# Optimization experiments

Hardware: AMD Instinct MI355X
Metric: run time of the kernel (lower is better)

## Reference

```python
import jax, jax.numpy as jnp
import numpy as np

N, E, D, K, H = 100000, 1600000, 32, 3, 1


def setup_inputs() -> dict:
    key = jax.random.key(0)
    ks = jax.random.split(key, 7)
    return {
        "src": jax.random.randint(ks[0], (E,), 0, N),
        "dst": jax.random.randint(ks[1], (E,), 0, N),
        "embedding": jax.random.normal(ks[2], (N, D), jnp.float32),
        "lambda_max": jnp.full((1,), 2.0, jnp.float32),
        # ChebConv: single Linear(k*d -> d) over concatenated Chebyshev terms (shared by both calls)
        "cheb_W": jax.random.normal(ks[3], (K * D, D), jnp.float32) / np.sqrt(K * D),
        "cheb_b": jnp.zeros((D,), jnp.float32),
        # GATv2: fc_src / fc_dst Linear(d -> H*d) + attention vector (H, d)
        "gat_W_src": jax.random.normal(ks[4], (D, H * D), jnp.float32) / np.sqrt(D),
        "gat_b_src": jnp.zeros((H * D,), jnp.float32),
        "gat_W_dst": jax.random.normal(ks[5], (D, H * D), jnp.float32) / np.sqrt(D),
        "gat_b_dst": jnp.zeros((H * D,), jnp.float32),
        "gat_attn": jax.random.normal(ks[6], (H, D), jnp.float32) / np.sqrt(D),
    }


def _cheb(src, dst, feat, lam, W, b, n):
    # DGL ChebConv with lambda_max given; activation = leaky_relu (slope 0.01)
    deg = jnp.clip(jax.ops.segment_sum(jnp.ones(src.shape[0], feat.dtype), dst, num_segments=n), 1.0)
    dinv = deg[:, None] ** -0.5  # D^{-1/2}, (N,1)
    re_norm = 2.0 / lam[0]

    def unnL(f):  # D^{-1/2} A D^{-1/2} f
        return jax.ops.segment_sum((f * dinv)[src], dst, num_segments=n) * dinv

    X0 = feat
    X1 = -re_norm * unnL(X0) + X0 * (re_norm - 1.0)
    Xs = [X0, X1]
    for _ in range(2, K):
        Xi = -2.0 * re_norm * unnL(X1) + X1 * (2.0 * (re_norm - 1.0)) - X0
        Xs.append(Xi)
        X0, X1 = X1, Xi
    return jax.nn.leaky_relu(jnp.concatenate(Xs, axis=1) @ W + b, 0.01)


def _gatv2(src, dst, h, Ws, bs, Wd, bd, attn, n):
    Hh, Dd = attn.shape
    fs = (h @ Ws + bs).reshape(n, Hh, Dd)  # feat_src 'el'
    fd = (h @ Wd + bd).reshape(n, Hh, Dd)  # feat_dst 'er'
    e = jax.nn.leaky_relu(fs[src] + fd[dst], 0.2)        # (E,H,D), GATv2 negative_slope=0.2
    logits = jnp.einsum('ehd,hd->eh', e, attn)           # (E,H)
    m = jax.ops.segment_max(logits, dst, num_segments=n)  # per-dst softmax (edge_softmax)
    ex = jnp.exp(logits - m[dst])
    a = ex / jax.ops.segment_sum(ex, dst, num_segments=n)[dst]
    ft = jax.ops.segment_sum(fs[src] * a[..., None], dst, num_segments=n)  # (N,H,D)
    return jax.nn.leaky_relu(ft, 0.01)  # activation=F.leaky_relu


def reference(src, dst, embedding, lambda_max, cheb_W, cheb_b,
              gat_W_src, gat_b_src, gat_W_dst, gat_b_dst, gat_attn):
    n, d = embedding.shape
    h = _cheb(src, dst, embedding, lambda_max, cheb_W, cheb_b, n)
    h = _cheb(src, dst, h, lambda_max, cheb_W, cheb_b, n)
    out = _gatv2(src, dst, h, gat_W_src, gat_b_src, gat_W_dst, gat_b_dst, gat_attn, n)
    return out.reshape(-1, d)
```

## Files before the change

### kernel.cpp

```cpp
#include <hip/hip_runtime.h>

#define TPB 256
#define NB 512
#define CAPB 4096
#define CHUNK 4096
#define CAPS 5120

__global__ void k_zero_u(unsigned int* p, int n){
  int i = blockIdx.x*TPB + threadIdx.x;
  if(i < n) p[i] = 0u;
}

__global__ void k_scan1(const unsigned int* deg, unsigned int* ptr,
                        unsigned int* bsum, int N){
  __shared__ unsigned int s[TPB];
  int i = blockIdx.x*TPB + threadIdx.x;
  unsigned int v = (i < N) ? deg[i] : 0u;
  s[threadIdx.x] = v; __syncthreads();
  for(int off = 1; off < TPB; off <<= 1){
    unsigned int x = (threadIdx.x >= off) ? s[threadIdx.x - off] : 0u;
    __syncthreads();
    s[threadIdx.x] += x;
    __syncthreads();
  }
  if(i < N) ptr[i] = s[threadIdx.x] - v;
  if(threadIdx.x == TPB-1) bsum[blockIdx.x] = s[TPB-1];
}

__global__ void k_scan2(unsigned int* bsum, int nb){
  __shared__ unsigned int s[TPB];
  __shared__ unsigned int carry;
  if(threadIdx.x == 0) carry = 0u;
  __syncthreads();
  for(int base = 0; base < nb; base += TPB){
    int i = base + threadIdx.x;
    unsigned int v = (i < nb) ? bsum[i] : 0u;
    s[threadIdx.x] = v; __syncthreads();
    for(int off = 1; off < TPB; off <<= 1){
      unsigned int x = (threadIdx.x >= off) ? s[threadIdx.x - off] : 0u;
      __syncthreads();
      s[threadIdx.x] += x;
      __syncthreads();
    }
    if(i < nb) bsum[i] = s[threadIdx.x] - v + carry;
    __syncthreads();
    if(threadIdx.x == 0) carry += s[TPB-1];
    __syncthreads();
  }
}

__global__ void k_scan3(unsigned int* ptr, const unsigned int* bsum, int N, int E){
  int i = blockIdx.x*TPB + threadIdx.x;
  if(i < N) ptr[i] += bsum[blockIdx.x];
  if(i == 0) ptr[N] = (unsigned int)E;
}

__global__ __launch_bounds__(TPB) void k_bin1(const int* __restrict__ src,
    const int* __restrict__ dst,
    unsigned int* __restrict__ btail, unsigned int* __restrict__ binned,
    int E, int npb){
  __shared__ unsigned int hist[NB];
  __shared__ unsigned int lofs[NB];
  __shared__ unsigned int base[NB];
  __shared__ unsigned int s[TPB];
  __shared__ int2 stage[CHUNK];
  int t = threadIdx.x;
  for(int i = t; i < NB; i += TPB) hist[i] = 0u;
  __syncthreads();
  int e0 = blockIdx.x*CHUNK;
  int e1 = e0 + CHUNK; if(e1 > E) e1 = E;
  for(int e = e0 + t; e < e1; e += TPB)
    atomicAdd(&hist[dst[e]/npb], 1u);
  __syncthreads();
  unsigned int a0 = hist[2*t], a1 = hist[2*t+1];
  unsigned int tsum = a0 + a1;
  s[t] = tsum; __syncthreads();
  for(int off = 1; off < TPB; off <<= 1){
    unsigned int x = (t >= off) ? s[t - off] : 0u;
    __syncthreads();
    s[t] += x;
    __syncthreads();
  }
  unsigned int excl = s[t] - tsum;
  lofs[2*t]   = excl;
  lofs[2*t+1] = excl + a0;
  base[2*t]   = a0 ? atomicAdd(btail + 2*t,   a0) : 0u;
  base[2*t+1] = a1 ? atomicAdd(btail + 2*t+1, a1) : 0u;
  __syncthreads();
  hist[2*t]   = lofs[2*t];
  hist[2*t+1] = lofs[2*t+1];
  __syncthreads();
  for(int e = e0 + t; e < e1; e += TPB){
    int d = dst[e];
    int b = d / npb;
    unsigned int p = atomicAdd(&hist[b], 1u);
    stage[p] = make_int2(src[e], d);
  }
  __syncthreads();
  int tot = e1 - e0;
  for(int i = t; i < tot; i += TPB){
    int2 sd = stage[i];
    int b = sd.y / npb;
    unsigned int go = base[b] + ((unsigned)i - lofs[b]);
    if(go < (unsigned)CAPB)
      binned[(size_t)b*CAPB + go] = ((unsigned)sd.x << 8) | (unsigned)(sd.y - b*npb);
  }
}

__global__ __launch_bounds__(TPB) void k_cnt(const unsigned int* __restrict__ binned,
    const unsigned int* __restrict__ btail,
    unsigned int* __restrict__ deg, float* __restrict__ dinv, int npb, int N){
  __shared__ unsigned int c[TPB];
  int b = blockIdx.x;
  int n0 = b*npb;
  int t = threadIdx.x;
  c[t] = 0u;
  __syncthreads();
  unsigned int cnt = btail[b]; if(cnt > (unsigned)CAPB) cnt = CAPB;
  const unsigned int* eb = binned + (size_t)b*CAPB;
  for(unsigned int i = t; i < cnt; i += TPB)
    atomicAdd(&c[eb[i] & 255u], 1u);
  __syncthreads();
  int n = n0 + t;
  if(t < npb && n < N){
    unsigned int d = c[t];
    deg[n] = d;
    dinv[n] = 1.0f / sqrtf(fmaxf((float)d, 1.0f));
  }
}

__global__ __launch_bounds__(TPB) void k_bin2(const unsigned int* __restrict__ binned,
    const unsigned int* __restrict__ ptr, int* __restrict__ csr, int npb, int N){
  __shared__ unsigned int curs[256];
  __shared__ int stage[CAPS];
  int b = blockIdx.x;
  int n0 = b*npb; if(n0 >= N) return;
  int n1 = n0 + npb; if(n1 > N) n1 = N;
  int t = threadIdx.x;
  unsigned int segbase = ptr[n0];
  unsigned int seglen  = ptr[n1] - segbase;
  for(int i = n0 + t; i < n1; i += TPB) curs[i - n0] = ptr[i] - segbase;
  __syncthreads();
  unsigned int cnt = seglen < (unsigned)CAPB ? seglen : (unsigned)CAPB;
  const unsigned int* eb = binned + (size_t)b*CAPB;
  if(seglen <= (unsigned)CAPS){
    for(unsigned int i = t; i < cnt; i += TPB){
      unsigned int sd = eb[i];
      unsigned int p0 = atomicAdd(&curs[sd & 255u], 1u);
      stage[p0] = (int)(sd >> 8);
    }
    __syncthreads();
    for(unsigned int i = t; i < seglen; i += TPB) csr[segbase + i] = stage[i];
  } else {
    for(unsigned int i = t; i < cnt; i += TPB){
      unsigned int sd = eb[i];
      unsigned int p0 = atomicAdd(&curs[sd & 255u], 1u);
      csr[segbase + p0] = (int)(sd >> 8);
    }
  }
}

__device__ __forceinline__ float4 agg_gather4(const unsigned int* __restrict__ ptr,
    const int* __restrict__ csr,
    const float* __restrict__ X, const float* __restrict__ dinv, int t, int lane){
  int g  = lane >> 3;
  int f4 = (lane & 7) << 2;
  unsigned int p0 = ptr[t], p1 = ptr[t+1];
  float4 S0 = make_float4(0.f,0.f,0.f,0.f);
  float4 S1 = make_float4(0.f,0.f,0.f,0.f);
  for(unsigned int base = p0; base < p1; base += 32){
    int idx = 0; float dva = 0.f;
    unsigned int pos = base + (unsigned)lane;
    if(pos < p1){ idx = csr[pos]; dva = dinv[idx]; }
    unsigned int cnt = p1 - base; if(cnt > 32u) cnt = 32u;
    unsigned int rounds = (cnt + 3u) >> 2;
    for(unsigned int r = 0; r < rounds; r += 2){
      int el0 = (int)(r << 2) + g;
      int s0  = __shfl(idx, el0, 32);
      float d0 = __shfl(dva, el0, 32);
      const float4 x0 = *(const float4*)(X + (size_t)s0*32 + f4);
      if(r + 1 < rounds){
        int el1 = el0 + 4;
        int s1  = __shfl(idx, el1, 32);
        float d1 = __shfl(dva, el1, 32);
        const float4 x1 = *(const float4*)(X + (size_t)s1*32 + f4);
        S1.x += x1.x*d1; S1.y += x1.y*d1; S1.z += x1.z*d1; S1.w += x1.w*d1;
      }
      S0.x += x0.x*d0; S0.y += x0.y*d0; S0.z += x0.z*d0; S0.w += x0.w*d0;
    }
  }
  float4 S;
  S.x = S0.x + S1.x; S.y = S0.y + S1.y; S.z = S0.z + S1.z; S.w = S0.w + S1.w;
  S.x += __shfl_xor(S.x, 8, 32);  S.y += __shfl_xor(S.y, 8, 32);
  S.z += __shfl_xor(S.z, 8, 32);  S.w += __shfl_xor(S.w, 8, 32);
  S.x += __shfl_xor(S.x, 16, 32); S.y += __shfl_xor(S.y, 16, 32);
  S.z += __shfl_xor(S.z, 16, 32); S.w += __shfl_xor(S.w, 16, 32);
  return S;
}

__global__ __launch_bounds__(TPB) void k_cheb1(const unsigned int* __restrict__ ptr,
    const int* __restrict__ csr,
    const float* __restrict__ X0, const float* __restrict__ dinv,
    const float* __restrict__ lam, float* __restrict__ X1, int N){
  int t = blockIdx.x*8 + (threadIdx.x >> 5);
  if(t >= N) return;
  int lane = threadIdx.x & 31;
  float4 S = agg_gather4(ptr, csr, X0, dinv, t, lane);
  if((lane >> 3) != 0) return;
  int f4 = (lane & 7) << 2;
  float re = 2.0f / lam[0];
  float dt = dinv[t];
  size_t o = (size_t)t*32 + f4;
  const float4 x0 = *(const float4*)(X0 + o);
  float4 r;
  r.x = -re*(S.x*dt) + (re-1.0f)*x0.x;
  r.y = -re*(S.y*dt) + (re-1.0f)*x0.y;
  r.z = -re*(S.z*dt) + (re-1.0f)*x0.z;
  r.w = -re*(S.w*dt) + (re-1.0f)*x0.w;
  *(float4*)(X1 + o) = r;
}

__global__ __launch_bounds__(TPB) void k_cheb2(const unsigned int* __restrict__ ptr,
    const int* __restrict__ csr,
    const float* __restrict__ X0, const float* __restrict__ X1,
    const float* __restrict__ dinv, const float* __restrict__ lam,
    float* __restrict__ X2, int N){
  int t = blockIdx.x*8 + (threadIdx.x >> 5);
  if(t >= N) return;
  int lane = threadIdx.x & 31;
  float4 S = agg_gather4(ptr, csr, X1, dinv, t, lane);
  if((lane >> 3) != 0) return;
  int f4 = (lane & 7) << 2;
  float re = 2.0f / lam[0];
  float dt = dinv[t];
  size_t o = (size_t)t*32 + f4;
  const float4 x0 = *(const float4*)(X0 + o);
  const float4 x1 = *(const float4*)(X1 + o);
  float c1 = -2.0f*re, c2 = 2.0f*(re-1.0f);
  float4 r;
  r.x = c1*(S.x*dt) + c2*x1.x - x0.x;
  r.y = c1*(S.y*dt) + c2*x1.y - x0.y;
  r.z = c1*(S.z*dt) + c2*x1.z - x0.z;
  r.w = c1*(S.w*dt) + c2*x1.w - x0.w;
  *(float4*)(X2 + o) = r;
}

__global__ __launch_bounds__(TPB) void k_lin(const float* __restrict__ X0,
    const float* __restrict__ X1,
    const float* __restrict__ X2, const float* __restrict__ W,
    const float* __restrict__ b, float* __restrict__ out, int N){
  int n = blockIdx.x*TPB + threadIdx.x;
  if(n >= N) return;
  float acc[32];
  #pragma unroll
  for(int c = 0; c < 32; c++) acc[c] = b[c];
  const float* xs0 = X0 + (size_t)n*32;
  const float* xs1 = X1 + (size_t)n*32;
  const float* xs2 = X2 + (size_t)n*32;
  #pragma unroll
  for(int s3 = 0; s3 < 3; s3++){
    const float4* xp = (const float4*)(s3 == 0 ? xs0 : (s3 == 1 ? xs1 : xs2));
    #pragma unroll
    for(int q = 0; q < 8; q++){
      float4 xv = xp[q];
      const float* Wr = W + (size_t)(s3*32 + q*4)*32;
      #pragma unroll
      for(int c = 0; c < 32; c++)
        acc[c] += xv.x*Wr[c] + xv.y*Wr[32+c] + xv.z*Wr[64+c] + xv.w*Wr[96+c];
    }
  }
  float4* op = (float4*)(out + (size_t)n*32);
  #pragma unroll
  for(int q = 0; q < 8; q++){
    float4 v;
    float a;
    a = acc[4*q+0]; v.x = a > 0.f ? a : 0.01f*a;
    a = acc[4*q+1]; v.y = a > 0.f ? a : 0.01f*a;
    a = acc[4*q+2]; v.z = a > 0.f ? a : 0.01f*a;
    a = acc[4*q+3]; v.w = a > 0.f ? a : 0.01f*a;
    op[q] = v;
  }
}

__global__ __launch_bounds__(TPB) void k_fc(const float* __restrict__ h,
    const float* __restrict__ Wsr, const float* __restrict__ bsr,
    const float* __restrict__ Wds, const float* __restrict__ bds,
    float* __restrict__ fs, float* __restrict__ fd, int N){
  int n = blockIdx.x*TPB + threadIdx.x;
  if(n >= N) return;
  float as[32], ad[32];
  #pragma unroll
  for(int c = 0; c < 32; c++){ as[c] = bsr[c]; ad[c] = bds[c]; }
  const float4* xp = (const float4*)(h + (size_t)n*32);
  #pragma unroll
  for(int q = 0; q < 8; q++){
    float4 xv = xp[q];
    const float* Wr = Wsr + (size_t)(q*4)*32;
    const float* Vr = Wds + (size_t)(q*4)*32;
    #pragma unroll
    for(int c = 0; c < 32; c++){
      as[c] += xv.x*Wr[c] + xv.y*Wr[32+c] + xv.z*Wr[64+c] + xv.w*Wr[96+c];
      ad[c] += xv.x*Vr[c] + xv.y*Vr[32+c] + xv.z*Vr[64+c] + xv.w*Vr[96+c];
    }
  }
  float4* sp = (float4*)(fs + (size_t)n*32);
  float4* dp = (float4*)(fd + (size_t)n*32);
  #pragma unroll
  for(int q = 0; q < 8; q++){
    float4 v1, v2;
    v1.x = as[4*q+0]; v1.y = as[4*q+1]; v1.z = as[4*q+2]; v1.w = as[4*q+3];
    v2.x = ad[4*q+0]; v2.y = ad[4*q+1]; v2.z = ad[4*q+2]; v2.w = ad[4*q+3];
    sp[q] = v1;
    dp[q] = v2;
  }
}

__global__ __launch_bounds__(TPB) void k_gat(const unsigned int* __restrict__ ptr,
    const int* __restrict__ csr,
    const float* __restrict__ fs, const float* __restrict__ fd,
    const float* __restrict__ attn, float* __restrict__ out, int N){
  int t = blockIdx.x*8 + (threadIdx.x >> 5);
  if(t >= N) return;
  int lane = threadIdx.x & 31;
  int g  = lane >> 3;
  int f4 = (lane & 7) << 2;
  unsigned int p0 = ptr[t], p1 = ptr[t+1];
  const float4 fd4 = *(const float4*)(fd + (size_t)t*32 + f4);
  const float4 at4 = *(const float4*)(attn + f4);
  float m = -3.402823466e38f, den = 0.f;
  float4 acc = make_float4(0.f,0.f,0.f,0.f);
  for(unsigned int base = p0; base < p1; base += 32){
    int idx = 0;
    unsigned int pos = base + (unsigned)lane;
    if(pos < p1) idx = csr[pos];
    unsigned int cnt = p1 - base; if(cnt > 32u) cnt = 32u;
    unsigned int rounds = (cnt + 3u) >> 2;
    for(unsigned int r = 0; r < rounds; r++){
      int el = (int)(r << 2) + g;
      int s  = __shfl(idx, el, 32);
      const float4 f = *(const float4*)(fs + (size_t)s*32 + f4);
      float vx = f.x + fd4.x; vx = vx > 0.f ? vx : 0.2f*vx;
      float vy = f.y + fd4.y; vy = vy > 0.f ? vy : 0.2f*vy;
      float vz = f.z + fd4.z; vz = vz > 0.f ? vz : 0.2f*vz;
      float vw = f.w + fd4.w; vw = vw > 0.f ? vw : 0.2f*vw;
      float pl = vx*at4.x + vy*at4.y + vz*at4.z + vw*at4.w;
      pl += __shfl_xor(pl, 4, 32);
      pl += __shfl_xor(pl, 2, 32);
      pl += __shfl_xor(pl, 1, 32);
      if(el < (int)cnt){
        float mn = fmaxf(m, pl);
        float sc = __expf(m - mn);
        float e  = __expf(pl - mn);
        den = den*sc + e;
        acc.x = acc.x*sc + f.x*e;
        acc.y = acc.y*sc + f.y*e;
        acc.z = acc.z*sc + f.z*e;
        acc.w = acc.w*sc + f.w*e;
        m = mn;
      }
    }
  }
  #pragma unroll
  for(int off = 8; off <= 16; off <<= 1){
    float mo = __shfl_xor(m, off, 32);
    float do_ = __shfl_xor(den, off, 32);
    float ax = __shfl_xor(acc.x, off, 32);
    float ay = __shfl_xor(acc.y, off, 32);
    float az = __shfl_xor(acc.z, off, 32);
    float aw = __shfl_xor(acc.w, off, 32);
    float mn = fmaxf(m, mo);
    float a = __expf(m - mn), b = __expf(mo - mn);
    den = den*a + do_*b;
    acc.x = acc.x*a + ax*b;
    acc.y = acc.y*a + ay*b;
    acc.z = acc.z*a + az*b;
    acc.w = acc.w*a + aw*b;
    m = mn;
  }
  if(g != 0) return;
  float4 o = make_float4(0.f,0.f,0.f,0.f);
  if(den > 0.f){
    float inv = 1.0f / den;
    o.x = acc.x*inv; o.x = o.x > 0.f ? o.x : 0.01f*o.x;
    o.y = acc.y*inv; o.y = o.y > 0.f ? o.y : 0.01f*o.y;
    o.z = acc.z*inv; o.z = o.z > 0.f ? o.z : 0.01f*o.z;
    o.w = acc.w*inv; o.w = o.w > 0.f ? o.w : 0.01f*o.w;
  }
  *(float4*)(out + (size_t)t*32 + f4) = o;
}

extern "C" void kernel_launch(void* const* d_in, const int* in_sizes, int n_in,
                              void* d_out, int out_size, void* d_ws, size_t ws_size,
                              hipStream_t stream){
  const int*   src = (const int*)d_in[0];
  const int*   dst = (const int*)d_in[1];
  const float* emb = (const float*)d_in[2];
  const float* lam = (const float*)d_in[3];
  const float* cW  = (const float*)d_in[4];
  const float* cB  = (const float*)d_in[5];
  const float* gWs = (const float*)d_in[6];
  const float* gbs = (const float*)d_in[7];
  const float* gWd = (const float*)d_in[8];
  const float* gbd = (const float*)d_in[9];
  const float* gat = (const float*)d_in[10];
  const int E  = in_sizes[0];
  const int N  = in_sizes[2] / 32;
  const int NF = N * 32;
  const int npb = (N + NB - 1) / NB;

  int gN  = (N + TPB-1)/TPB;
  int gR  = (N + 7)/8;
  int gB1 = (E + CHUNK-1)/CHUNK;

  char* p = (char*)d_ws;
  auto alloc = [&](size_t bytes)->char*{ char* r = p; p += (bytes + 255) & ~(size_t)255; return r; };
  unsigned int* degi = (unsigned int*)alloc((size_t)N*4);
  unsigned int* ptrA = (unsigned int*)alloc((size_t)(N+1)*4);
  unsigned int* btail= (unsigned int*)alloc((size_t)NB*4);
  unsigned int* bsum = (unsigned int*)alloc((size_t)(gN+1)*4);
  float* dinv = (float*)alloc((size_t)N*4);
  int*   csr  = (int*)alloc((size_t)E*4);
  float* X1   = (float*)alloc((size_t)NF*4);
  float* X2   = (float*)alloc((size_t)NF*4);
  float* h1   = (float*)alloc((size_t)NF*4);
  float* h2   = (float*)alloc((size_t)NF*4);
  unsigned int* binned = (unsigned int*)X1;

  k_zero_u<<<(NB+TPB-1)/TPB, TPB, 0, stream>>>(btail, NB);
  k_bin1<<<gB1, TPB, 0, stream>>>(src, dst, btail, binned, E, npb);
  k_cnt<<<NB, TPB, 0, stream>>>(binned, btail, degi, dinv, npb, N);
  k_scan1<<<gN, TPB, 0, stream>>>(degi, ptrA, bsum, N);
  k_scan2<<<1,  TPB, 0, stream>>>(bsum, gN);
  k_scan3<<<gN, TPB, 0, stream>>>(ptrA, bsum, N, E);
  k_bin2<<<NB,  TPB, 0, stream>>>(binned, ptrA, csr, npb, N);

  k_cheb1<<<gR, TPB, 0, stream>>>(ptrA, csr, emb, dinv, lam, X1, N);
  k_cheb2<<<gR, TPB, 0, stream>>>(ptrA, csr, emb, X1, dinv, lam, X2, N);
  k_lin<<<gN, TPB, 0, stream>>>(emb, X1, X2, cW, cB, h1, N);

  k_cheb1<<<gR, TPB, 0, stream>>>(ptrA, csr, h1, dinv, lam, X1, N);
  k_cheb2<<<gR, TPB, 0, stream>>>(ptrA, csr, h1, X1, dinv, lam, X2, N);
  k_lin<<<gN, TPB, 0, stream>>>(h1, X1, X2, cW, cB, h2, N);

  k_fc<<<gN, TPB, 0, stream>>>(h2, gWs, gbs, gWd, gbd, X1 , X2 , N);
  k_gat<<<gR, TPB, 0, stream>>>(ptrA, csr, X1, X2, gat, (float*)d_out, N);
}
```

Before: 385.6 us.

## Fuse degree count, scan and CSR scatter into bucket-level scan plus one kernel

Replaces the per-node degree kernel, three-pass global scan and separate CSR fill with a single-block scan over bucket totals followed by one kernel per bucket. That kernel stages the bucket's edges in shared memory, counts degrees, does a local scan, and writes ptr, dinv and the CSR. This removes three launches and a round trip of degree and ptr data through global memory during graph preprocessing. The cost is more shared memory per block (about 34 KB), which may lower occupancy, and bucket overflow beyond CAPB is still handled by truncation.

```diff
diff --git a/kernel.cpp b/kernel.cpp
--- a/kernel.cpp
+++ b/kernel.cpp
@@ -4,55 +4,10 @@
 #define NB 512
 #define CAPB 4096
 #define CHUNK 4096
-#define CAPS 5120
 
 __global__ void k_zero_u(unsigned int* p, int n){
   int i = blockIdx.x*TPB + threadIdx.x;
   if(i < n) p[i] = 0u;
-}
-
-__global__ void k_scan1(const unsigned int* deg, unsigned int* ptr,
-                        unsigned int* bsum, int N){
-  __shared__ unsigned int s[TPB];
-  int i = blockIdx.x*TPB + threadIdx.x;
-  unsigned int v = (i < N) ? deg[i] : 0u;
-  s[threadIdx.x] = v; __syncthreads();
-  for(int off = 1; off < TPB; off <<= 1){
-    unsigned int x = (threadIdx.x >= off) ? s[threadIdx.x - off] : 0u;
-    __syncthreads();
-    s[threadIdx.x] += x;
-    __syncthreads();
-  }
-  if(i < N) ptr[i] = s[threadIdx.x] - v;
-  if(threadIdx.x == TPB-1) bsum[blockIdx.x] = s[TPB-1];
-}
-
-__global__ void k_scan2(unsigned int* bsum, int nb){
-  __shared__ unsigned int s[TPB];
-  __shared__ unsigned int carry;
-  if(threadIdx.x == 0) carry = 0u;
-  __syncthreads();
-  for(int base = 0; base < nb; base += TPB){
-    int i = base + threadIdx.x;
-    unsigned int v = (i < nb) ? bsum[i] : 0u;
-    s[threadIdx.x] = v; __syncthreads();
-    for(int off = 1; off < TPB; off <<= 1){
-      unsigned int x = (threadIdx.x >= off) ? s[threadIdx.x - off] : 0u;
-      __syncthreads();
-      s[threadIdx.x] += x;
-      __syncthreads();
-    }
-    if(i < nb) bsum[i] = s[threadIdx.x] - v + carry;
-    __syncthreads();
-    if(threadIdx.x == 0) carry += s[TPB-1];
-    __syncthreads();
-  }
-}
-
-__global__ void k_scan3(unsigned int* ptr, const unsigned int* bsum, int N, int E){
-  int i = blockIdx.x*TPB + threadIdx.x;
-  if(i < N) ptr[i] += bsum[blockIdx.x];
-  if(i == 0) ptr[N] = (unsigned int)E;
 }
 
 __global__ __launch_bounds__(TPB) void k_bin1(const int* __restrict__ src,
@@ -107,57 +62,76 @@
   }
 }
 
-__global__ __launch_bounds__(TPB) void k_cnt(const unsigned int* __restrict__ binned,
-    const unsigned int* __restrict__ btail,
-    unsigned int* __restrict__ deg, float* __restrict__ dinv, int npb, int N){
-  __shared__ unsigned int c[TPB];
+__global__ __launch_bounds__(TPB) void k_scanb(const unsigned int* __restrict__ btail,
+    unsigned int* __restrict__ bbase, unsigned int* __restrict__ ptr, int N, int E){
+  __shared__ unsigned int s[TPB];
+  __shared__ unsigned int carry;
+  int t = threadIdx.x;
+  if(t == 0) carry = 0u;
+  __syncthreads();
+  for(int base = 0; base < NB; base += TPB){
+    unsigned int v = btail[base + t];
+    s[t] = v; __syncthreads();
+    for(int off = 1; off < TPB; off <<= 1){
+      unsigned int x = (t >= off) ? s[t - off] : 0u;
+      __syncthreads();
+      s[t] += x;
+      __syncthreads();
+    }
+    bbase[base + t] = s[t] - v + carry;
+    __syncthreads();
+    if(t == 0) carry += s[TPB-1];
+    __syncthreads();
+  }
+  if(t == 0) ptr[N] = (unsigned int)E;
+}
+
+__global__ __launch_bounds__(TPB) void k_bin2x(const unsigned int* __restrict__ binned,
+    const unsigned int* __restrict__ btail, const unsigned int* __restrict__ bbase,
+    unsigned int* __restrict__ ptr, float* __restrict__ dinv,
+    int* __restrict__ csr, int npb, int N){
+  __shared__ unsigned int ebuf[CAPB];
+  __shared__ int obuf[CAPB];
+  __shared__ unsigned int cnt_s[256];
+  __shared__ unsigned int s[TPB];
+  __shared__ unsigned int curs[256];
   int b = blockIdx.x;
-  int n0 = b*npb;
+  int n0 = b*npb; if(n0 >= N) return;
   int t = threadIdx.x;
-  c[t] = 0u;
-  __syncthreads();
   unsigned int cnt = btail[b]; if(cnt > (unsigned)CAPB) cnt = CAPB;
-  const unsigned int* eb = binned + (size_t)b*CAPB;
-  for(unsigned int i = t; i < cnt; i += TPB)
-    atomicAdd(&c[eb[i] & 255u], 1u);
-  __syncthreads();
+  unsigned int segbase = bbase[b];
+  cnt_s[t] = 0u;
+  __syncthreads();
+  for(unsigned int i = t; i < cnt; i += TPB){
+    unsigned int e = binned[(size_t)b*CAPB + i];
+    ebuf[i] = e;
+    atomicAdd(&cnt_s[e & 255u], 1u);
+  }
+  __syncthreads();
+  unsigned int v = cnt_s[t];
+  s[t] = v; __syncthreads();
+  for(int off = 1; off < TPB; off <<= 1){
+    unsigned int x = (t >= off) ? s[t - off] : 0u;
+    __syncthreads();
+    s[t] += x;
+    __syncthreads();
+  }
+  unsigned int lo = s[t] - v;
   int n = n0 + t;
   if(t < npb && n < N){
-    unsigned int d = c[t];
-    deg[n] = d;
-    dinv[n] = 1.0f / sqrtf(fmaxf((float)d, 1.0f));
-  }
-}
-
-__global__ __launch_bounds__(TPB) void k_bin2(const unsigned int* __restrict__ binned,
-    const unsigned int* __restrict__ ptr, int* __restrict__ csr, int npb, int N){
-  __shared__ unsigned int curs[256];
-  __shared__ int stage[CAPS];
-  int b = blockIdx.x;
-  int n0 = b*npb; if(n0 >= N) return;
-  int n1 = n0 + npb; if(n1 > N) n1 = N;
-  int t = threadIdx.x;
-  unsigned int segbase = ptr[n0];
-  unsigned int seglen  = ptr[n1] - segbase;
-  for(int i = n0 + t; i < n1; i += TPB) curs[i - n0] = ptr[i] - segbase;
-  __syncthreads();
-  unsigned int cnt = seglen < (unsigned)CAPB ? seglen : (unsigned)CAPB;
-  const unsigned int* eb = binned + (size_t)b*CAPB;
-  if(seglen <= (unsigned)CAPS){
-    for(unsigned int i = t; i < cnt; i += TPB){
-      unsigned int sd = eb[i];
-      unsigned int p0 = atomicAdd(&curs[sd & 255u], 1u);
-      stage[p0] = (int)(sd >> 8);
-    }
-    __syncthreads();
-    for(unsigned int i = t; i < seglen; i += TPB) csr[segbase + i] = stage[i];
-  } else {
-    for(unsigned int i = t; i < cnt; i += TPB){
-      unsigned int sd = eb[i];
-      unsigned int p0 = atomicAdd(&curs[sd & 255u], 1u);
-      csr[segbase + p0] = (int)(sd >> 8);
-    }
-  }
+    ptr[n]  = segbase + lo;
+    dinv[n] = 1.0f / sqrtf(fmaxf((float)v, 1.0f));
+  }
+  curs[t] = lo;
+  __syncthreads();
+  for(unsigned int i = t; i < cnt; i += TPB){
+    unsigned int e = ebuf[i];
+    unsigned int p = atomicAdd(&curs[e & 255u], 1u);
+    obuf[p] = (int)(e >> 8);
+  }
+  __syncthreads();
+  for(unsigned int i = t; i < cnt; i += TPB)
+    csr[segbase + i] = obuf[i];
 }
 
 __device__ __forceinline__ float4 agg_gather4(const unsigned int* __restrict__ ptr,
@@ -414,10 +388,9 @@
 
   char* p = (char*)d_ws;
   auto alloc = [&](size_t bytes)->char*{ char* r = p; p += (bytes + 255) & ~(size_t)255; return r; };
-  unsigned int* degi = (unsigned int*)alloc((size_t)N*4);
   unsigned int* ptrA = (unsigned int*)alloc((size_t)(N+1)*4);
   unsigned int* btail= (unsigned int*)alloc((size_t)NB*4);
-  unsigned int* bsum = (unsigned int*)alloc((size_t)(gN+1)*4);
+  unsigned int* bbase= (unsigned int*)alloc((size_t)NB*4);
   float* dinv = (float*)alloc((size_t)N*4);
   int*   csr  = (int*)alloc((size_t)E*4);
   float* X1   = (float*)alloc((size_t)NF*4);
@@ -428,11 +401,8 @@
 
   k_zero_u<<<(NB+TPB-1)/TPB, TPB, 0, stream>>>(btail, NB);
   k_bin1<<<gB1, TPB, 0, stream>>>(src, dst, btail, binned, E, npb);
-  k_cnt<<<NB, TPB, 0, stream>>>(binned, btail, degi, dinv, npb, N);
-  k_scan1<<<gN, TPB, 0, stream>>>(degi, ptrA, bsum, N);
-  k_scan2<<<1,  TPB, 0, stream>>>(bsum, gN);
-  k_scan3<<<gN, TPB, 0, stream>>>(ptrA, bsum, N, E);
-  k_bin2<<<NB,  TPB, 0, stream>>>(binned, ptrA, csr, npb, N);
+  k_scanb<<<1, TPB, 0, stream>>>(btail, bbase, ptrA, N, E);
+  k_bin2x<<<NB, TPB, 0, stream>>>(binned, btail, bbase, ptrA, dinv, csr, npb, N);
 
   k_cheb1<<<gR, TPB, 0, stream>>>(ptrA, csr, emb, dinv, lam, X1, N);
   k_cheb2<<<gR, TPB, 0, stream>>>(ptrA, csr, emb, X1, dinv, lam, X2, N);
```

Measured after the change: 376.4 us. 1.02x faster.
